# Performance work log

Hardware: AMD Instinct MI355X
Metric: run time of the kernel (lower is better)

The kernel has to match this reference:

```python
import jax, jax.numpy as jnp
import numpy as np

HID, NL, NH, DH, FF = 768, 12, 12, 64, 3072
VOCAB, MAXPOS = 30522, 512
T_ELE, T_ROLE = 17, 7
B, L = 16, 256
LN_EPS = 1e-12


def _layernorm(x, g, b):
    mu = x.mean(-1, keepdims=True)
    var = ((x - mu) ** 2).mean(-1, keepdims=True)
    return (x - mu) / jnp.sqrt(var + LN_EPS) * g + b


def _bert(datas, word_emb, pos_emb, type_emb, emb_ln_g, emb_ln_b,
          Wq, bq, Wk, bk, Wv, bv, Wo, bo, ln1_g, ln1_b,
          W1, b1, W2, b2, ln2_g, ln2_b):
    Bv, Lv = datas.shape
    x = word_emb[datas] + pos_emb[:Lv][None] + type_emb[0][None, None]
    x = _layernorm(x, emb_ln_g, emb_ln_b)
    for i in range(NL):  # loop over fixed layer count, not data dims
        q = (x @ Wq[i] + bq[i]).reshape(Bv, Lv, NH, DH)
        k = (x @ Wk[i] + bk[i]).reshape(Bv, Lv, NH, DH)
        v = (x @ Wv[i] + bv[i]).reshape(Bv, Lv, NH, DH)
        att = jax.nn.softmax(jnp.einsum('bqhd,bkhd->bhqk', q, k) / jnp.sqrt(jnp.float32(DH)), axis=-1)
        ctx = jnp.einsum('bhqk,bkhd->bqhd', att, v).reshape(Bv, Lv, HID)
        x = _layernorm(x + ctx @ Wo[i] + bo[i], ln1_g[i], ln1_b[i])
        h = jax.nn.gelu(x @ W1[i] + b1[i], approximate=False)
        x = _layernorm(x + h @ W2[i] + b2[i], ln2_g[i], ln2_b[i])
    return x


def _crf_llh(em, tags, mask, start, end, trans):
    # torchcrf CRF.forward with batch_first=True, reduction='sum'
    Bv, Lv, T = em.shape
    bidx = jnp.arange(Bv)
    em_t = jnp.transpose(em, (1, 0, 2))        # [L,B,T]
    tags_t = tags.T.astype(jnp.int32)          # [L,B]
    mask_t = mask.T.astype(em.dtype)           # [L,B]
    # numerator: score of gold path
    score = start[tags_t[0]] + em_t[0][bidx, tags_t[0]]
    def num_step(s, xs):
        e_t, tg, tp, m = xs
        return s + m * (trans[tp, tg] + e_t[bidx, tg]), None
    score, _ = jax.lax.scan(num_step, score, (em_t[1:], tags_t[1:], tags_t[:-1], mask_t[1:]))
    last_idx = (mask_t.sum(0) - 1).astype(jnp.int32)
    num = score + end[tags[bidx, last_idx]]
    # denominator: forward algorithm (log-sum-exp semiring)
    alpha = start[None] + em_t[0]              # [B,T]
    def den_step(a, xs):
        e_t, m = xs
        nxt = jax.nn.logsumexp(a[:, :, None] + trans[None] + e_t[:, None, :], axis=1)
        return jnp.where(m[:, None] > 0, nxt, a), None
    alpha, _ = jax.lax.scan(den_step, alpha, (em_t[1:], mask_t[1:]))
    den = jax.nn.logsumexp(alpha + end[None], axis=1)
    return jnp.sum(num - den)


def _crf_decode(em, start, end, trans):
    # torchcrf CRF.decode without mask -> full-length Viterbi
    Bv = em.shape[0]
    bidx = jnp.arange(Bv)
    em_t = jnp.transpose(em, (1, 0, 2))        # [L,B,T]
    alpha = start[None] + em_t[0]
    def fwd(a, e_t):
        sc = a[:, :, None] + trans[None]       # [B,T_prev,T_cur]
        return jnp.max(sc, axis=1) + e_t, jnp.argmax(sc, axis=1)
    alpha, hist = jax.lax.scan(fwd, alpha, em_t[1:])   # hist [L-1,B,T]
    last = jnp.argmax(alpha + end[None], axis=1)
    def back(cur, h):
        prev = h[bidx, cur]
        return prev, prev
    _, ys = jax.lax.scan(back, last, hist, reverse=True)  # ys[t] = tag at pos t
    return jnp.concatenate([ys, last[None]], axis=0).T    # [B,L]


def setup_inputs() -> dict:
    key = jax.random.key(0)
    ks = iter(jax.random.split(key, 64))
    n = lambda shape: jax.random.normal(next(ks), shape, dtype=jnp.float32) * 0.02
    inp = {
        'datas': jax.random.randint(next(ks), (B, L), 0, VOCAB, dtype=jnp.int32),
        'ele_labels': jax.random.randint(next(ks), (B, L), 0, T_ELE, dtype=jnp.int32),
        'role_labels': jax.random.randint(next(ks), (B, L), 0, T_ROLE, dtype=jnp.int32),
        'seq_mask': jnp.ones((B, L), dtype=bool),
        'word_emb': n((VOCAB, HID)), 'pos_emb': n((MAXPOS, HID)), 'type_emb': n((2, HID)),
        'emb_ln_g': jnp.ones((HID,)), 'emb_ln_b': jnp.zeros((HID,)),
        'Wq': n((NL, HID, HID)), 'bq': jnp.zeros((NL, HID)),
        'Wk': n((NL, HID, HID)), 'bk': jnp.zeros((NL, HID)),
        'Wv': n((NL, HID, HID)), 'bv': jnp.zeros((NL, HID)),
        'Wo': n((NL, HID, HID)), 'bo': jnp.zeros((NL, HID)),
        'ln1_g': jnp.ones((NL, HID)), 'ln1_b': jnp.zeros((NL, HID)),
        'W1': n((NL, HID, FF)), 'b1': jnp.zeros((NL, FF)),
        'W2': n((NL, FF, HID)), 'b2': jnp.zeros((NL, HID)),
        'ln2_g': jnp.ones((NL, HID)), 'ln2_b': jnp.zeros((NL, HID)),
        'W_ele': n((HID, T_ELE)), 'b_ele': jnp.zeros((T_ELE,)),
        'W_role': n((HID, T_ROLE)), 'b_role': jnp.zeros((T_ROLE,)),
        'ele_start': n((T_ELE,)), 'ele_end': n((T_ELE,)), 'ele_trans': n((T_ELE, T_ELE)),
        'role_start': n((T_ROLE,)), 'role_end': n((T_ROLE,)), 'role_trans': n((T_ROLE, T_ROLE)),
    }
    return inp


def reference(datas, ele_labels, role_labels, seq_mask,
              word_emb, pos_emb, type_emb, emb_ln_g, emb_ln_b,
              Wq, bq, Wk, bk, Wv, bv, Wo, bo, ln1_g, ln1_b,
              W1, b1, W2, b2, ln2_g, ln2_b,
              W_ele, b_ele, W_role, b_role,
              ele_start, ele_end, ele_trans, role_start, role_end, role_trans):
    wemb = _bert(datas, word_emb, pos_emb, type_emb, emb_ln_g, emb_ln_b,
                 Wq, bq, Wk, bk, Wv, bv, Wo, bo, ln1_g, ln1_b,
                 W1, b1, W2, b2, ln2_g, ln2_b)
    ele_em = wemb @ W_ele + b_ele
    role_em = wemb @ W_role + b_role
    mask = seq_mask.astype(jnp.float32)
    ele_llh = _crf_llh(ele_em, ele_labels, mask, ele_start, ele_end, ele_trans)
    role_llh = _crf_llh(role_em, role_labels, mask, role_start, role_end, role_trans)
    loss = -ele_llh - role_llh
    ele_dec = _crf_decode(ele_em, ele_start, ele_end, ele_trans)
    role_dec = _crf_decode(role_em, role_start, role_end, role_trans)
    return loss, ele_dec, role_dec
```

## Files before the change

### kernel.cpp

```cpp
#include <hip/hip_runtime.h>
#include <stdint.h>
#include <math.h>

typedef _Float16 f16;
typedef _Float16 f16x8 __attribute__((ext_vector_type(8)));
typedef float f32x4 __attribute__((ext_vector_type(4)));

#define LO_SCALE 2048.0f
#define INV_LO_SCALE (1.0f/2048.0f)
#define LOG2E 1.4426950408889634f
#define MFMA16(a, b, c) __builtin_amdgcn_mfma_f32_16x16x32_f16(a, b, c, 0, 0, 0)

__device__ __forceinline__ void split1(float x, f16 &hi, f16 &lo) {
    f16 h = (f16)x;
    hi = h;
    lo = (f16)((x - (float)h) * LO_SCALE);
}

__device__ __forceinline__ float fexp2(float x) {
#if __has_builtin(__builtin_amdgcn_exp2f)
    return __builtin_amdgcn_exp2f(x);
#else
    return exp2f(x);
#endif
}
__device__ __forceinline__ float flog2(float x) {
#if __has_builtin(__builtin_amdgcn_logf)
    return __builtin_amdgcn_logf(x);
#else
    return log2f(x);
#endif
}

#define GLOAD16(g, l) __builtin_amdgcn_global_load_lds( \
    (const __attribute__((address_space(1))) void*)(g), \
    (__attribute__((address_space(3))) void*)(l), 16, 0, 0)

template<int EPI>
__global__ __launch_bounds__(256, 2)
void gemm_split(const f16* __restrict__ Ah, const f16* __restrict__ Al,
                const f16* __restrict__ Bh, const f16* __restrict__ Bl,
                const float* __restrict__ bias, float* __restrict__ C,
                f16* __restrict__ Oh, f16* __restrict__ Ol,
                f16* __restrict__ X2h, f16* __restrict__ X2l,
                f16* __restrict__ X3h, f16* __restrict__ X3l, int K, int N)
{
    __shared__ f16 smem[2][16384];

    const int m0 = blockIdx.x * 128;
    const int n0 = blockIdx.y * 128;
    const int tid = threadIdx.x;
    const int lane = tid & 63;
    const int w = tid >> 6;
    const int wr = (w >> 1) * 64;
    const int wc = (w & 1) * 64;

    f32x4 accm[4][4];
    f32x4 accc[4][4];
#pragma unroll
    for (int i = 0; i < 4; ++i)
#pragma unroll
        for (int j = 0; j < 4; ++j) {
            accm[i][j] = (f32x4){0.f, 0.f, 0.f, 0.f};
            accc[i][j] = (f32x4){0.f, 0.f, 0.f, 0.f};
        }

    const int srow = lane & 15;
    const int skb = lane >> 4;
    const f16* gA0 = Ah + (size_t)(m0 + w * 32 + srow) * K + skb * 8;
    const f16* gA1 = gA0 + 16 * (size_t)K;
    const f16* gCl0 = Al + (size_t)(m0 + w * 32 + srow) * K + skb * 8;
    const f16* gCl1 = gCl0 + 16 * (size_t)K;
    const f16* gB0 = Bh + (size_t)(n0 + w * 32 + srow) * K + skb * 8;
    const f16* gB1 = gB0 + 16 * (size_t)K;
    const f16* gDl0 = Bl + (size_t)(n0 + w * 32 + srow) * K + skb * 8;
    const f16* gDl1 = gDl0 + 16 * (size_t)K;
    const int ldsb0 = w * 1024;
    const int ldsb1 = w * 1024 + 512;

    const int r16 = lane & 15;
    const int kb = lane >> 4;
    const int wrg = (w >> 1) * 4;
    const int wcg = (w & 1) * 4;

    const int nt = K >> 5;

#define STAGE(buf, k0)                                   \
    {                                                    \
        f16* sb = &smem[buf][0];                         \
        GLOAD16(gA0 + (k0), sb + ldsb0);                 \
        GLOAD16(gA1 + (k0), sb + ldsb1);                 \
        GLOAD16(gCl0 + (k0), sb + 4096 + ldsb0);         \
        GLOAD16(gCl1 + (k0), sb + 4096 + ldsb1);         \
        GLOAD16(gB0 + (k0), sb + 8192 + ldsb0);          \
        GLOAD16(gB1 + (k0), sb + 8192 + ldsb1);          \
        GLOAD16(gDl0 + (k0), sb + 12288 + ldsb0);        \
        GLOAD16(gDl1 + (k0), sb + 12288 + ldsb1);        \
    }

    STAGE(0, 0);
    __syncthreads();

    int cur = 0;
    for (int t = 0; t < nt; ++t) {
        if (t + 1 < nt) STAGE(cur ^ 1, (t + 1) * 32);

        const f16* sb = &smem[cur][0];
        f16x8 fah[4], fal[4], fbh[4], fbl[4];
#pragma unroll
        for (int mi = 0; mi < 4; ++mi) {
            int offa = (wrg + mi) * 512 + kb * 128 + r16 * 8;
            fah[mi] = *(const f16x8*)(sb + offa);
            fal[mi] = *(const f16x8*)(sb + 4096 + offa);
            int offb = (wcg + mi) * 512 + kb * 128 + r16 * 8;
            fbh[mi] = *(const f16x8*)(sb + 8192 + offb);
            fbl[mi] = *(const f16x8*)(sb + 12288 + offb);
        }
#pragma unroll
        for (int mi = 0; mi < 4; ++mi)
#pragma unroll
            for (int ni = 0; ni < 4; ++ni) {
                accm[mi][ni] = MFMA16(fah[mi], fbh[ni], accm[mi][ni]);
                accc[mi][ni] = MFMA16(fah[mi], fbl[ni], accc[mi][ni]);
                accc[mi][ni] = MFMA16(fal[mi], fbh[ni], accc[mi][ni]);
            }

        __syncthreads();
        cur ^= 1;
    }
#undef STAGE

#pragma unroll
    for (int mi = 0; mi < 4; ++mi) {
        int row = m0 + wr + mi * 16 + (lane >> 4) * 4;
#pragma unroll
        for (int ni = 0; ni < 4; ++ni) {
            int col = n0 + wc + ni * 16 + (lane & 15);
            float bv = bias[col];
#pragma unroll
            for (int j = 0; j < 4; ++j) {
                float val = accm[mi][ni][j] + accc[mi][ni][j] * INV_LO_SCALE + bv;
                if constexpr (EPI == 0) {
                    C[(size_t)(row + j) * N + col] = val;
                } else if constexpr (EPI == 1) {
                    float ge = 0.5f * val * (1.0f + erff(val * 0.70710678118654752440f));
                    f16 hi, lo;
                    split1(ge, hi, lo);
                    size_t o = (size_t)(row + j) * N + col;
                    Oh[o] = hi;
                    Ol[o] = lo;
                } else {
                    int sect = col >= 1536 ? 2 : (col >= 768 ? 1 : 0);
                    int cc = col - sect * 768;
                    int hd = cc >> 6;
                    int d = cc & 63;
                    int rr = row + j;
                    int bh = (rr >> 8) * 12 + hd;
                    int lt = rr & 255;
                    f16 hi, lo;
                    split1(val, hi, lo);
                    if (sect == 0) {
                        size_t o = ((size_t)bh * 256 + lt) * 64 + d;
                        Oh[o] = hi; Ol[o] = lo;
                    } else if (sect == 1) {
                        size_t o = ((size_t)bh * 256 + lt) * 64 + d;
                        X2h[o] = hi; X2l[o] = lo;
                    } else {
                        size_t o = ((size_t)bh * 64 + d) * 256 + lt;
                        X3h[o] = hi; X3l[o] = lo;
                    }
                }
            }
        }
    }
}

__global__ __launch_bounds__(256, 1)
void attn_mfma_kernel(const f16* __restrict__ Qh, const f16* __restrict__ Ql,
                      const f16* __restrict__ Kh, const f16* __restrict__ Kl,
                      const f16* __restrict__ Vth, const f16* __restrict__ Vtl,
                      f16* __restrict__ ch, f16* __restrict__ cl)
{
    __shared__ f16 sKh[256 * 72];
    __shared__ f16 sKl[256 * 72];
    __shared__ f16 sVh[64 * 264];
    __shared__ f16 sVl[64 * 264];
    __shared__ f16 sPh[4][1280];
    __shared__ f16 sPl[4][1280];

    const int bh = blockIdx.x >> 1;
    const int qbase = (blockIdx.x & 1) * 128;
    const int b = bh / 12;
    const int h = bh % 12;
    const int tid = threadIdx.x;
    const int w = tid >> 6;
    const int l = tid & 63;
    const int l15 = l & 15;
    const int lg = l >> 4;

    {
        const f16* gKh = Kh + (size_t)bh * 16384;
        const f16* gKl = Kl + (size_t)bh * 16384;
#pragma unroll
        for (int i = 0; i < 8; ++i) {
            int c = tid + i * 256;
            int off = (c >> 3) * 72 + (c & 7) * 8;
            *(f16x8*)(sKh + off) = *(const f16x8*)(gKh + c * 8);
            *(f16x8*)(sKl + off) = *(const f16x8*)(gKl + c * 8);
        }
        const f16* gVh = Vth + (size_t)bh * 16384;
        const f16* gVl = Vtl + (size_t)bh * 16384;
#pragma unroll
        for (int i = 0; i < 8; ++i) {
            int c = tid + i * 256;
            int off = (c >> 5) * 264 + (c & 31) * 8;
            *(f16x8*)(sVh + off) = *(const f16x8*)(gVh + c * 8);
            *(f16x8*)(sVl + off) = *(const f16x8*)(gVl + c * 8);
        }
    }
    __syncthreads();

    f16x8 qfh[2][2], qfl[2][2];
#pragma unroll
    for (int mt = 0; mt < 2; ++mt) {
        int qr = qbase + w * 32 + mt * 16 + l15;
        size_t qo = ((size_t)bh * 256 + qr) * 64 + lg * 8;
        qfh[mt][0] = *(const f16x8*)(Qh + qo);
        qfh[mt][1] = *(const f16x8*)(Qh + qo + 32);
        qfl[mt][0] = *(const f16x8*)(Ql + qo);
        qfl[mt][1] = *(const f16x8*)(Ql + qo + 32);
    }

    f32x4 S[2][16];
#pragma unroll
    for (int nt = 0; nt < 16; ++nt) {
        int kr = nt * 16 + l15;
        int kaddr = kr * 72 + lg * 8;
        f16x8 kh0 = *(const f16x8*)(sKh + kaddr);
        f16x8 kh1 = *(const f16x8*)(sKh + kaddr + 32);
        f16x8 kl0 = *(const f16x8*)(sKl + kaddr);
        f16x8 kl1 = *(const f16x8*)(sKl + kaddr + 32);
#pragma unroll
        for (int mt = 0; mt < 2; ++mt) {
            f32x4 am = (f32x4){0.f, 0.f, 0.f, 0.f};
            f32x4 ac = (f32x4){0.f, 0.f, 0.f, 0.f};
            am = MFMA16(qfh[mt][0], kh0, am);
            am = MFMA16(qfh[mt][1], kh1, am);
            ac = MFMA16(qfh[mt][0], kl0, ac);
            ac = MFMA16(qfh[mt][1], kl1, ac);
            ac = MFMA16(qfl[mt][0], kh0, ac);
            ac = MFMA16(qfl[mt][1], kh1, ac);
            S[mt][nt] = (am + ac * INV_LO_SCALE) * 0.125f;
        }
    }

#pragma unroll
    for (int mt = 0; mt < 2; ++mt)
#pragma unroll
        for (int j = 0; j < 4; ++j) {
            float m = S[mt][0][j];
#pragma unroll
            for (int nt = 1; nt < 16; ++nt) m = fmaxf(m, S[mt][nt][j]);
            m = fmaxf(m, __shfl_xor(m, 1));
            m = fmaxf(m, __shfl_xor(m, 2));
            m = fmaxf(m, __shfl_xor(m, 4));
            m = fmaxf(m, __shfl_xor(m, 8));
            float s = 0.f;
#pragma unroll
            for (int nt = 0; nt < 16; ++nt) {
                float e = fexp2((S[mt][nt][j] - m) * LOG2E);
                S[mt][nt][j] = e;
                s += e;
            }
            s += __shfl_xor(s, 1);
            s += __shfl_xor(s, 2);
            s += __shfl_xor(s, 4);
            s += __shfl_xor(s, 8);
            float inv = 1.0f / s;
#pragma unroll
            for (int nt = 0; nt < 16; ++nt) S[mt][nt][j] *= inv;
        }

    f32x4 Ohh[2][4], Occ[2][4];
#pragma unroll
    for (int mt = 0; mt < 2; ++mt)
#pragma unroll
        for (int dt = 0; dt < 4; ++dt) {
            Ohh[mt][dt] = (f32x4){0.f, 0.f, 0.f, 0.f};
            Occ[mt][dt] = (f32x4){0.f, 0.f, 0.f, 0.f};
        }

    f16* pbh = &sPh[w][0];
    f16* pbl = &sPl[w][0];
#pragma unroll
    for (int kp = 0; kp < 8; ++kp) {
#pragma unroll
        for (int mt = 0; mt < 2; ++mt)
#pragma unroll
            for (int n2 = 0; n2 < 2; ++n2) {
                int nt = kp * 2 + n2;
#pragma unroll
                for (int j = 0; j < 4; ++j) {
                    int prow = mt * 16 + lg * 4 + j;
                    int pcol = n2 * 16 + l15;
                    f16 hi, lo;
                    split1(S[mt][nt][j], hi, lo);
                    pbh[prow * 40 + pcol] = hi;
                    pbl[prow * 40 + pcol] = lo;
                }
            }
        __builtin_amdgcn_wave_barrier();
#pragma unroll
        for (int mt = 0; mt < 2; ++mt) {
            int paddr = (mt * 16 + l15) * 40 + lg * 8;
            f16x8 ph = *(const f16x8*)(pbh + paddr);
            f16x8 pl = *(const f16x8*)(pbl + paddr);
#pragma unroll
            for (int dt = 0; dt < 4; ++dt) {
                int vaddr = (dt * 16 + l15) * 264 + kp * 32 + lg * 8;
                f16x8 vh = *(const f16x8*)(sVh + vaddr);
                f16x8 vl = *(const f16x8*)(sVl + vaddr);
                Ohh[mt][dt] = MFMA16(ph, vh, Ohh[mt][dt]);
                Occ[mt][dt] = MFMA16(ph, vl, Occ[mt][dt]);
                Occ[mt][dt] = MFMA16(pl, vh, Occ[mt][dt]);
            }
        }
        __builtin_amdgcn_wave_barrier();
    }

#pragma unroll
    for (int mt = 0; mt < 2; ++mt)
#pragma unroll
        for (int dt = 0; dt < 4; ++dt) {
            f32x4 o = Ohh[mt][dt] + Occ[mt][dt] * INV_LO_SCALE;
#pragma unroll
            for (int j = 0; j < 4; ++j) {
                int q = qbase + w * 32 + mt * 16 + lg * 4 + j;
                int d = dt * 16 + l15;
                size_t off = ((size_t)(b * 256 + q)) * 768 + h * 64 + d;
                f16 hi, lo;
                split1(o[j], hi, lo);
                ch[off] = hi;
                cl[off] = lo;
            }
        }
}

__device__ __forceinline__ void tsplit_tile(const float* __restrict__ W,
                                            f16* __restrict__ Th, f16* __restrict__ Tl,
                                            int K, int N, int kb, int nb, int tid,
                                            float (*tile)[33])
{
    const int k0 = kb * 32;
    const int n0 = nb * 32;
    const int r = tid >> 3;
    const int c4 = (tid & 7) * 4;
    float4 v = *(const float4*)&W[(size_t)(k0 + r) * N + n0 + c4];
    tile[r][c4 + 0] = v.x; tile[r][c4 + 1] = v.y;
    tile[r][c4 + 2] = v.z; tile[r][c4 + 3] = v.w;
    __syncthreads();
    f16 hs[4], ls[4];
#pragma unroll
    for (int j = 0; j < 4; ++j) split1(tile[c4 + j][r], hs[j], ls[j]);
    size_t o = (size_t)(n0 + r) * K + k0 + c4;
    Th[o + 0] = hs[0]; Th[o + 1] = hs[1]; Th[o + 2] = hs[2]; Th[o + 3] = hs[3];
    Tl[o + 0] = ls[0]; Tl[o + 1] = ls[1]; Tl[o + 2] = ls[2]; Tl[o + 3] = ls[3];
}

__global__ void tsplit_all_kernel(const float* __restrict__ Wq, const float* __restrict__ Wk,
                                  const float* __restrict__ Wv, const float* __restrict__ Wo,
                                  const float* __restrict__ W1, const float* __restrict__ W2,
                                  f16* __restrict__ qkvh, f16* __restrict__ qkvl,
                                  f16* __restrict__ woh, f16* __restrict__ wol,
                                  f16* __restrict__ w1h, f16* __restrict__ w1l,
                                  f16* __restrict__ w2h, f16* __restrict__ w2l)
{
    __shared__ float tile[32][33];
    const int tid = threadIdx.x;
    int bid = blockIdx.x;
    if (bid < 576) {
        tsplit_tile(Wq, qkvh, qkvl, 768, 768, bid % 24, bid / 24, tid, tile);
    } else if (bid < 1152) {
        bid -= 576;
        tsplit_tile(Wk, qkvh + 768 * 768, qkvl + 768 * 768, 768, 768, bid % 24, bid / 24, tid, tile);
    } else if (bid < 1728) {
        bid -= 1152;
        tsplit_tile(Wv, qkvh + 2 * 768 * 768, qkvl + 2 * 768 * 768, 768, 768, bid % 24, bid / 24, tid, tile);
    } else if (bid < 2304) {
        bid -= 1728;
        tsplit_tile(Wo, woh, wol, 768, 768, bid % 24, bid / 24, tid, tile);
    } else if (bid < 4608) {
        bid -= 2304;
        tsplit_tile(W1, w1h, w1l, 768, 3072, bid % 24, bid / 24, tid, tile);
    } else {
        bid -= 4608;
        tsplit_tile(W2, w2h, w2l, 3072, 768, bid % 96, bid / 96, tid, tile);
    }
}

__global__ void pack_qkv_bias_kernel(const float* __restrict__ bq, const float* __restrict__ bk,
                                     const float* __restrict__ bv, float* __restrict__ qkvb)
{
    const int i = blockIdx.x;
    const int tid = threadIdx.x;
    for (int c = tid; c < 768; c += 256) {
        qkvb[i * 2304 + c]        = bq[i * 768 + c];
        qkvb[i * 2304 + 768 + c]  = bk[i * 768 + c];
        qkvb[i * 2304 + 1536 + c] = bv[i * 768 + c];
    }
}

__device__ void ln_emit(float* vals, float* red, const float* __restrict__ g,
                        const float* __restrict__ be, float* xout,
                        f16* oh, f16* ol, size_t base, int tid)
{
    float s = vals[tid] + vals[tid + 256] + vals[tid + 512];
    red[tid] = s;
    __syncthreads();
    for (int st = 128; st > 0; st >>= 1) { if (tid < st) red[tid] += red[tid + st]; __syncthreads(); }
    float mu = red[0] * (1.0f / 768.0f);
    __syncthreads();
    float d0 = vals[tid] - mu, d1 = vals[tid + 256] - mu, d2 = vals[tid + 512] - mu;
    red[tid] = d0 * d0 + d1 * d1 + d2 * d2;
    __syncthreads();
    for (int st = 128; st > 0; st >>= 1) { if (tid < st) red[tid] += red[tid + st]; __syncthreads(); }
    float var = red[0] * (1.0f / 768.0f);
    float rstd = 1.0f / sqrtf(var + 1e-12f);
    __syncthreads();
    for (int c = tid; c < 768; c += 256) {
        float o = (vals[c] - mu) * rstd * g[c] + be[c];
        if (xout) xout[base + c] = o;
        f16 hi, lo;
        split1(o, hi, lo);
        oh[base + c] = hi;
        ol[base + c] = lo;
    }
}

__global__ void embed_ln_kernel(const int* __restrict__ datas, const float* __restrict__ wemb,
                                const float* __restrict__ pemb, const float* __restrict__ temb,
                                const float* __restrict__ g, const float* __restrict__ be,
                                float* __restrict__ x, f16* __restrict__ xh, f16* __restrict__ xl)
{
    __shared__ float vals[768];
    __shared__ float red[256];
    const int i = blockIdx.x;
    const int tid = threadIdx.x;
    const int l = i & 255;
    const int widx = datas[i];
    for (int c = tid; c < 768; c += 256)
        vals[c] = wemb[(size_t)widx * 768 + c] + pemb[(size_t)l * 768 + c] + temb[c];
    __syncthreads();
    ln_emit(vals, red, g, be, x, xh, xl, (size_t)i * 768, tid);
}

__global__ void res_ln_kernel(float* __restrict__ x, const float* __restrict__ y,
                              const float* __restrict__ g, const float* __restrict__ be,
                              f16* __restrict__ xh, f16* __restrict__ xl)
{
    __shared__ float vals[768];
    __shared__ float red[256];
    const int i = blockIdx.x;
    const int tid = threadIdx.x;
    const size_t base = (size_t)i * 768;
    for (int c = tid; c < 768; c += 256) vals[c] = x[base + c] + y[base + c];
    __syncthreads();
    ln_emit(vals, red, g, be, x, xh, xl, base, tid);
}

__global__ void head_kernel(const float* __restrict__ X, const float* __restrict__ Wh,
                            const float* __restrict__ bh, float* __restrict__ out, int T)
{
    __shared__ float xs[768];
    __shared__ double part[8][32];
    const int i = blockIdx.x;
    const int tid = threadIdx.x;
    for (int c = tid; c < 768; c += 256) xs[c] = X[(size_t)i * 768 + c];
    __syncthreads();
    const int p = tid >> 5;
    const int tg = tid & 31;
    if (tg < T) {
        double a = 0;
        for (int d = p * 96; d < p * 96 + 96; ++d)
            a += (double)xs[d] * (double)Wh[d * T + tg];
        part[p][tg] = a;
    }
    __syncthreads();
    if (tid < T) {
        double s = 0;
        for (int pp = 0; pp < 8; ++pp) s += part[pp][tid];
        out[(size_t)i * T + tid] = (float)(s + (double)bh[tid]);
    }
}

__global__ void crf_num_kernel(const float* __restrict__ em, const int* __restrict__ labels,
                               const float* __restrict__ start, const float* __restrict__ endv,
                               const float* __restrict__ trans, float* __restrict__ num, int T)
{
    __shared__ double red[256];
    const int b = blockIdx.x;
    const int tid = threadIdx.x;
    const int tag = labels[b * 256 + tid];
    float v;
    if (tid == 0) {
        v = start[tag] + em[(size_t)(b * 256) * T + tag];
    } else {
        int pt = labels[b * 256 + tid - 1];
        v = trans[pt * T + tag] + em[(size_t)(b * 256 + tid) * T + tag];
    }
    red[tid] = (double)v;
    __syncthreads();
    for (int st = 128; st > 0; st >>= 1) { if (tid < st) red[tid] += red[tid + st]; __syncthreads(); }
    if (tid == 0) num[b] = (float)(red[0] + (double)endv[labels[b * 256 + 255]]);
}

template<int T>
__global__ void crf_scan_kernel(const float* __restrict__ emG, const float* __restrict__ start,
                                const float* __restrict__ endv, const float* __restrict__ trans,
                                float* __restrict__ den, float* __restrict__ tagOut)
{
    __shared__ float ems[256 * T];
    __shared__ float albuf[32];
    __shared__ unsigned char hist[255 * T + 1];
    const int b = blockIdx.x;
    const bool vit = (blockIdx.y == 1);
    const int c = threadIdx.x;

    for (int idx = c; idx < 256 * T; idx += 64)
        ems[idx] = emG[(size_t)b * 256 * T + idx];
    float trc[T];
#pragma unroll
    for (int p = 0; p < T; ++p) trc[p] = (c < T) ? trans[p * T + c] : 0.f;
    const float ec = (c < T) ? endv[c] : -1e30f;
    __syncthreads();

    float alpha = (c < T) ? (start[c] + ems[c]) : -1e30f;

    if (!vit) {
        for (int t = 1; t < 256; ++t) {
            if (c < T) albuf[c] = alpha;
            __builtin_amdgcn_wave_barrier();
            float a[T];
            float m = -1e30f;
#pragma unroll
            for (int p = 0; p < T; ++p) { a[p] = albuf[p] + trc[p]; m = fmaxf(m, a[p]); }
            float s = 0.f;
#pragma unroll
            for (int p = 0; p < T; ++p) s += fexp2((a[p] - m) * LOG2E);
            float na = m + flog2(s) * 0.6931471805599453f + ems[t * T + c];
            __builtin_amdgcn_wave_barrier();
            if (c < T) alpha = na;
        }
        if (c < T) albuf[c] = alpha + ec;
        __builtin_amdgcn_wave_barrier();
        if (c == 0) {
            float m = -1e30f;
            for (int p = 0; p < T; ++p) m = fmaxf(m, albuf[p]);
            float s = 0.f;
            for (int p = 0; p < T; ++p) s += fexp2((albuf[p] - m) * LOG2E);
            den[b] = m + flog2(s) * 0.6931471805599453f;
        }
    } else {
        for (int t = 1; t < 256; ++t) {
            if (c < T) albuf[c] = alpha;
            __builtin_amdgcn_wave_barrier();
            float best = albuf[0] + trc[0];
            int arg = 0;
#pragma unroll
            for (int p = 1; p < T; ++p) {
                float v2 = albuf[p] + trc[p];
                if (v2 > best) { best = v2; arg = p; }
            }
            __builtin_amdgcn_wave_barrier();
            if (c < T) {
                alpha = best + ems[t * T + c];
                hist[(t - 1) * T + c] = (unsigned char)arg;
            }
        }
        if (c < T) albuf[c] = alpha + ec;
        __builtin_amdgcn_wave_barrier();
        if (c == 0) {
            float bv = albuf[0];
            int cur = 0;
            for (int p = 1; p < T; ++p) {
                if (albuf[p] > bv) { bv = albuf[p]; cur = p; }
            }
            tagOut[b * 256 + 255] = (float)cur;
            for (int t = 254; t >= 0; --t) {
                cur = hist[t * T + cur];
                tagOut[b * 256 + t] = (float)cur;
            }
        }
    }
}

__global__ void loss_kernel(const float* __restrict__ num, const float* __restrict__ den,
                            float* __restrict__ out)
{
    __shared__ double red[32];
    const int tid = threadIdx.x;
    red[tid] = (double)num[tid] - (double)den[tid];
    __syncthreads();
    for (int st = 16; st > 0; st >>= 1) { if (tid < st) red[tid] += red[tid + st]; __syncthreads(); }
    if (tid == 0) out[0] = (float)(-red[0]);
}

extern "C" void kernel_launch(void* const* d_in, const int* in_sizes, int n_in,
                              void* d_out, int out_size, void* d_ws, size_t ws_size,
                              hipStream_t stream)
{
    (void)in_sizes; (void)n_in; (void)out_size; (void)ws_size;
    const int* datas       = (const int*)d_in[0];
    const int* ele_labels  = (const int*)d_in[1];
    const int* role_labels = (const int*)d_in[2];
    const float* word_emb = (const float*)d_in[4];
    const float* pos_emb  = (const float*)d_in[5];
    const float* type_emb = (const float*)d_in[6];
    const float* emb_g = (const float*)d_in[7];
    const float* emb_b = (const float*)d_in[8];
    const float* Wq = (const float*)d_in[9];  const float* bq = (const float*)d_in[10];
    const float* Wk = (const float*)d_in[11]; const float* bk = (const float*)d_in[12];
    const float* Wv = (const float*)d_in[13]; const float* bv = (const float*)d_in[14];
    const float* Wo = (const float*)d_in[15]; const float* bo = (const float*)d_in[16];
    const float* ln1g = (const float*)d_in[17]; const float* ln1b = (const float*)d_in[18];
    const float* W1 = (const float*)d_in[19]; const float* b1 = (const float*)d_in[20];
    const float* W2 = (const float*)d_in[21]; const float* b2 = (const float*)d_in[22];
    const float* ln2g = (const float*)d_in[23]; const float* ln2b = (const float*)d_in[24];
    const float* W_ele = (const float*)d_in[25]; const float* b_ele = (const float*)d_in[26];
    const float* W_role = (const float*)d_in[27]; const float* b_role = (const float*)d_in[28];
    const float* ele_start = (const float*)d_in[29];
    const float* ele_end   = (const float*)d_in[30];
    const float* ele_trans = (const float*)d_in[31];
    const float* role_start = (const float*)d_in[32];
    const float* role_end   = (const float*)d_in[33];
    const float* role_trans = (const float*)d_in[34];
    float* out = (float*)d_out;

    uint8_t* ws = (uint8_t*)d_ws;
    float* x      = (float*)(ws + 0x0000000);
    f16* xh       = (f16*)  (ws + 0x0C00000);
    f16* xl       = (f16*)  (ws + 0x1200000);
    f16* Qh       = (f16*)  (ws + 0x1800000);
    f16* Ql       = (f16*)  (ws + 0x1E00000);
    f16* Kh       = (f16*)  (ws + 0x2400000);
    f16* Kl       = (f16*)  (ws + 0x2A00000);
    f16* Vth      = (f16*)  (ws + 0x3000000);
    f16* Vtl      = (f16*)  (ws + 0x3600000);
    f16* ctxh     = (f16*)  (ws + 0x3C00000);
    f16* ctxl     = (f16*)  (ws + 0x4200000);
    float* rbuf   = (float*)(ws + 0x4800000);
    f16* hh       = (f16*)  (ws + 0x1800000);
    f16* hl       = (f16*)  (ws + 0x3000000);
    f16* wqkv_h   = (f16*)  (ws + 0x5400000);
    f16* wqkv_l   = (f16*)  (ws + 0x5760000);
    f16* wo_h     = (f16*)  (ws + 0x5AC0000);
    f16* wo_l     = (f16*)  (ws + 0x5BE0000);
    f16* w1_h     = (f16*)  (ws + 0x5D00000);
    f16* w1_l     = (f16*)  (ws + 0x6180000);
    f16* w2_h     = (f16*)  (ws + 0x6600000);
    f16* w2_l     = (f16*)  (ws + 0x6A80000);
    float* qkvb   = (float*)(ws + 0x6F00000);
    float* ele_em = (float*)(ws + 0x6F20000);
    float* role_em= (float*)(ws + 0x6F70000);
    float* numb   = (float*)(ws + 0x6FC0000);
    float* denb   = (float*)(ws + 0x6FC0100);

    pack_qkv_bias_kernel<<<12, 256, 0, stream>>>(bq, bk, bv, qkvb);
    embed_ln_kernel<<<4096, 256, 0, stream>>>(datas, word_emb, pos_emb, type_emb,
                                              emb_g, emb_b, x, xh, xl);

    for (int i = 0; i < 12; ++i) {
        const size_t o768 = (size_t)i * 768 * 768;
        const size_t o3072 = (size_t)i * 768 * 3072;
        tsplit_all_kernel<<<6912, 256, 0, stream>>>(Wq + o768, Wk + o768, Wv + o768, Wo + o768,
                                                    W1 + o3072, W2 + o3072,
                                                    wqkv_h, wqkv_l, wo_h, wo_l,
                                                    w1_h, w1_l, w2_h, w2_l);
        gemm_split<2><<<dim3(32, 18), 256, 0, stream>>>(xh, xl, wqkv_h, wqkv_l,
                                                        qkvb + i * 2304, nullptr,
                                                        Qh, Ql, Kh, Kl, Vth, Vtl, 768, 2304);
        attn_mfma_kernel<<<384, 256, 0, stream>>>(Qh, Ql, Kh, Kl, Vth, Vtl, ctxh, ctxl);
        gemm_split<0><<<dim3(32, 6), 256, 0, stream>>>(ctxh, ctxl, wo_h, wo_l,
                                                       bo + i * 768, rbuf, nullptr, nullptr,
                                                       nullptr, nullptr, nullptr, nullptr, 768, 768);
        res_ln_kernel<<<4096, 256, 0, stream>>>(x, rbuf, ln1g + i * 768, ln1b + i * 768, xh, xl);
        gemm_split<1><<<dim3(32, 24), 256, 0, stream>>>(xh, xl, w1_h, w1_l,
                                                        b1 + i * 3072, nullptr, hh, hl,
                                                        nullptr, nullptr, nullptr, nullptr, 768, 3072);
        gemm_split<0><<<dim3(32, 6), 256, 0, stream>>>(hh, hl, w2_h, w2_l,
                                                       b2 + i * 768, rbuf, nullptr, nullptr,
                                                       nullptr, nullptr, nullptr, nullptr, 3072, 768);
        res_ln_kernel<<<4096, 256, 0, stream>>>(x, rbuf, ln2g + i * 768, ln2b + i * 768, xh, xl);
    }

    head_kernel<<<4096, 256, 0, stream>>>(x, W_ele, b_ele, ele_em, 17);
    head_kernel<<<4096, 256, 0, stream>>>(x, W_role, b_role, role_em, 7);

    crf_num_kernel<<<16, 256, 0, stream>>>(ele_em, ele_labels, ele_start, ele_end, ele_trans, numb, 17);
    crf_num_kernel<<<16, 256, 0, stream>>>(role_em, role_labels, role_start, role_end, role_trans, numb + 16, 7);
    crf_scan_kernel<17><<<dim3(16, 2), 64, 0, stream>>>(ele_em, ele_start, ele_end, ele_trans, denb, out + 1);
    crf_scan_kernel<7><<<dim3(16, 2), 64, 0, stream>>>(role_em, role_start, role_end, role_trans, denb + 16, out + 1 + 4096);
    loss_kernel<<<1, 32, 0, stream>>>(numb, denb, out);
}
```

Baseline: 5.931 ms.

## Add 256x128-tile triple-buffered GEMM for QKV and FFN1 with XCD-aware block remap

Adds a new 512-thread GEMM kernel with a 256x128 output tile, a three-stage LDS ring fed by global_load_lds, staggered prefetch interleaved with the MFMA loop, and s_setprio around the MFMA bursts. It is used for the QKV and FFN-up projections in place of the 128x128 double-buffered kernel, aiming for more operand reuse per block and better hiding of load latency. The existing kernel also gains a blockIdx remap that spreads neighbouring tiles across the eight XCDs for L2 locality. The risks are lower occupancy from the large LDS footprint and one block per CU, and fewer blocks in the grid.

```diff
diff --git a/kernel.cpp b/kernel.cpp
--- a/kernel.cpp
+++ b/kernel.cpp
@@ -35,6 +35,177 @@
 #define GLOAD16(g, l) __builtin_amdgcn_global_load_lds( \
     (const __attribute__((address_space(1))) void*)(g), \
     (__attribute__((address_space(3))) void*)(l), 16, 0, 0)
+
+template<int EPI>
+__device__ __forceinline__ void epi_write(float val, int row, int col, int N,
+                                          float* __restrict__ C,
+                                          f16* __restrict__ Oh, f16* __restrict__ Ol,
+                                          f16* __restrict__ X2h, f16* __restrict__ X2l,
+                                          f16* __restrict__ X3h, f16* __restrict__ X3l)
+{
+    if constexpr (EPI == 0) {
+        C[(size_t)row * N + col] = val;
+    } else if constexpr (EPI == 1) {
+        float ge = 0.5f * val * (1.0f + erff(val * 0.70710678118654752440f));
+        f16 hi, lo;
+        split1(ge, hi, lo);
+        size_t o = (size_t)row * N + col;
+        Oh[o] = hi;
+        Ol[o] = lo;
+    } else {
+        int sect = col >= 1536 ? 2 : (col >= 768 ? 1 : 0);
+        int cc = col - sect * 768;
+        int hd = cc >> 6;
+        int d = cc & 63;
+        int bh = (row >> 8) * 12 + hd;
+        int lt = row & 255;
+        f16 hi, lo;
+        split1(val, hi, lo);
+        if (sect == 0) {
+            size_t o = ((size_t)bh * 256 + lt) * 64 + d;
+            Oh[o] = hi; Ol[o] = lo;
+        } else if (sect == 1) {
+            size_t o = ((size_t)bh * 256 + lt) * 64 + d;
+            X2h[o] = hi; X2l[o] = lo;
+        } else {
+            size_t o = ((size_t)bh * 64 + d) * 256 + lt;
+            X3h[o] = hi; X3l[o] = lo;
+        }
+    }
+}
+
+template<int EPI>
+__global__ __launch_bounds__(512, 1)
+void gemm256(const f16* __restrict__ Ah, const f16* __restrict__ Al,
+             const f16* __restrict__ Bh, const f16* __restrict__ Bl,
+             const float* __restrict__ bias, float* __restrict__ C,
+             f16* __restrict__ Oh, f16* __restrict__ Ol,
+             f16* __restrict__ X2h, f16* __restrict__ X2l,
+             f16* __restrict__ X3h, f16* __restrict__ X3l, int K, int N)
+{
+    __shared__ f16 smem[3][24576];
+
+    const int nwg = (N >> 7) << 4;
+    int s = blockIdx.x + blockIdx.y * 16;
+    const int q = nwg >> 3;
+    int wg = (s & 7) * q + (s >> 3);
+    const int m0 = (wg & 15) * 256;
+    const int n0 = (wg >> 4) * 128;
+
+    const int tid = threadIdx.x;
+    const int w = tid >> 6;
+    const int lane = tid & 63;
+    const int l15 = lane & 15;
+    const int lg = lane >> 4;
+
+    f32x4 accm[4][4];
+    f32x4 accc[4][4];
+#pragma unroll
+    for (int i = 0; i < 4; ++i)
+#pragma unroll
+        for (int j = 0; j < 4; ++j) {
+            accm[i][j] = (f32x4){0.f, 0.f, 0.f, 0.f};
+            accc[i][j] = (f32x4){0.f, 0.f, 0.f, 0.f};
+        }
+
+    const int r0 = m0 + w * 32 + l15;
+    const int c0 = n0 + w * 16 + l15;
+    const f16* gAh0 = Ah + (size_t)r0 * K + lg * 8;
+    const f16* gAh1 = gAh0 + 16 * (size_t)K;
+    const f16* gAl0 = Al + (size_t)r0 * K + lg * 8;
+    const f16* gAl1 = gAl0 + 16 * (size_t)K;
+    const f16* gBh0 = Bh + (size_t)c0 * K + lg * 8;
+    const f16* gBl0 = Bl + (size_t)c0 * K + lg * 8;
+
+    const int nt = K >> 5;
+    const int fro = lg * 128 + l15 * 8;
+
+    {
+        f16* sb = &smem[0][0];
+        GLOAD16(gAh0, sb + w * 1024);
+        GLOAD16(gAl0, sb + 8192 + w * 1024);
+        GLOAD16(gAh1, sb + w * 1024 + 512);
+        GLOAD16(gAl1, sb + 8192 + w * 1024 + 512);
+        GLOAD16(gBh0, sb + 16384 + w * 512);
+        GLOAD16(gBl0, sb + 20480 + w * 512);
+        sb = &smem[1][0];
+        GLOAD16(gAh0 + 32, sb + w * 1024);
+        GLOAD16(gAl0 + 32, sb + 8192 + w * 1024);
+        GLOAD16(gAh1 + 32, sb + w * 1024 + 512);
+        GLOAD16(gAl1 + 32, sb + 8192 + w * 1024 + 512);
+        GLOAD16(gBh0 + 32, sb + 16384 + w * 512);
+        GLOAD16(gBl0 + 32, sb + 20480 + w * 512);
+    }
+
+    int bt = 0;
+    for (int t = 0; t < nt; ++t) {
+        if (t + 1 < nt) {
+            asm volatile("s_waitcnt vmcnt(6)" ::: "memory");
+        } else {
+            asm volatile("s_waitcnt vmcnt(0)" ::: "memory");
+        }
+        __builtin_amdgcn_s_barrier();
+        __builtin_amdgcn_sched_barrier(0);
+
+        const f16* sb = &smem[bt][0];
+        int bs = bt + 2; if (bs >= 3) bs -= 3;
+        f16* sb2 = &smem[bs][0];
+        const bool doStage = (t + 2 < nt);
+        const int k2 = (t + 2) * 32;
+
+        f16x8 fbh[4], fbl[4];
+#pragma unroll
+        for (int ni = 0; ni < 4; ++ni) {
+            int g = (w & 1) * 4 + ni;
+            fbh[ni] = *(const f16x8*)(sb + 16384 + g * 512 + fro);
+            fbl[ni] = *(const f16x8*)(sb + 20480 + g * 512 + fro);
+        }
+#pragma unroll
+        for (int mt = 0; mt < 4; ++mt) {
+            if (doStage) {
+                if (mt == 0) {
+                    GLOAD16(gAh0 + k2, sb2 + w * 1024);
+                    GLOAD16(gAl0 + k2, sb2 + 8192 + w * 1024);
+                } else if (mt == 1) {
+                    GLOAD16(gAh1 + k2, sb2 + w * 1024 + 512);
+                    GLOAD16(gAl1 + k2, sb2 + 8192 + w * 1024 + 512);
+                } else if (mt == 2) {
+                    GLOAD16(gBh0 + k2, sb2 + 16384 + w * 512);
+                    GLOAD16(gBl0 + k2, sb2 + 20480 + w * 512);
+                }
+            }
+            int ga = (w >> 1) * 4 + mt;
+            f16x8 fah = *(const f16x8*)(sb + ga * 512 + fro);
+            f16x8 fal = *(const f16x8*)(sb + 8192 + ga * 512 + fro);
+            __builtin_amdgcn_s_setprio(1);
+#pragma unroll
+            for (int ni = 0; ni < 4; ++ni) {
+                accm[mt][ni] = MFMA16(fah, fbh[ni], accm[mt][ni]);
+                accc[mt][ni] = MFMA16(fah, fbl[ni], accc[mt][ni]);
+                accc[mt][ni] = MFMA16(fal, fbh[ni], accc[mt][ni]);
+            }
+            __builtin_amdgcn_s_setprio(0);
+        }
+        bt = bt + 1; if (bt >= 3) bt = 0;
+    }
+
+    const int wr = (w >> 1) * 64;
+    const int wc = (w & 1) * 64;
+#pragma unroll
+    for (int mt = 0; mt < 4; ++mt) {
+        int row = m0 + wr + mt * 16 + lg * 4;
+#pragma unroll
+        for (int ni = 0; ni < 4; ++ni) {
+            int col = n0 + wc + ni * 16 + l15;
+            float bv = bias[col];
+#pragma unroll
+            for (int j = 0; j < 4; ++j) {
+                float val = accm[mt][ni][j] + accc[mt][ni][j] * INV_LO_SCALE + bv;
+                epi_write<EPI>(val, row + j, col, N, C, Oh, Ol, X2h, X2l, X3h, X3l);
+            }
+        }
+    }
+}
 
 template<int EPI>
 __global__ __launch_bounds__(256, 2)
@@ -47,8 +218,16 @@
 {
     __shared__ f16 smem[2][16384];
 
-    const int m0 = blockIdx.x * 128;
-    const int n0 = blockIdx.y * 128;
+    const int nwg = gridDim.x * gridDim.y;
+    int s = blockIdx.x + blockIdx.y * gridDim.x;
+    int wg = s;
+    if ((nwg & 7) == 0) {
+        int q = nwg >> 3;
+        wg = (s & 7) * q + (s >> 3);
+    }
+    const int m0 = (wg % gridDim.x) * 128;
+    const int n0 = (wg / gridDim.x) * 128;
+
     const int tid = threadIdx.x;
     const int lane = tid & 63;
     const int w = tid >> 6;
@@ -140,36 +319,7 @@
 #pragma unroll
             for (int j = 0; j < 4; ++j) {
                 float val = accm[mi][ni][j] + accc[mi][ni][j] * INV_LO_SCALE + bv;
-                if constexpr (EPI == 0) {
-                    C[(size_t)(row + j) * N + col] = val;
-                } else if constexpr (EPI == 1) {
-                    float ge = 0.5f * val * (1.0f + erff(val * 0.70710678118654752440f));
-                    f16 hi, lo;
-                    split1(ge, hi, lo);
-                    size_t o = (size_t)(row + j) * N + col;
-                    Oh[o] = hi;
-                    Ol[o] = lo;
-                } else {
-                    int sect = col >= 1536 ? 2 : (col >= 768 ? 1 : 0);
-                    int cc = col - sect * 768;
-                    int hd = cc >> 6;
-                    int d = cc & 63;
-                    int rr = row + j;
-                    int bh = (rr >> 8) * 12 + hd;
-                    int lt = rr & 255;
-                    f16 hi, lo;
-                    split1(val, hi, lo);
-                    if (sect == 0) {
-                        size_t o = ((size_t)bh * 256 + lt) * 64 + d;
-                        Oh[o] = hi; Ol[o] = lo;
-                    } else if (sect == 1) {
-                        size_t o = ((size_t)bh * 256 + lt) * 64 + d;
-                        X2h[o] = hi; X2l[o] = lo;
-                    } else {
-                        size_t o = ((size_t)bh * 64 + d) * 256 + lt;
-                        X3h[o] = hi; X3l[o] = lo;
-                    }
-                }
+                epi_write<EPI>(val, row + j, col, N, C, Oh, Ol, X2h, X2l, X3h, X3l);
             }
         }
     }
@@ -676,17 +826,17 @@
                                                     W1 + o3072, W2 + o3072,
                                                     wqkv_h, wqkv_l, wo_h, wo_l,
                                                     w1_h, w1_l, w2_h, w2_l);
-        gemm_split<2><<<dim3(32, 18), 256, 0, stream>>>(xh, xl, wqkv_h, wqkv_l,
-                                                        qkvb + i * 2304, nullptr,
-                                                        Qh, Ql, Kh, Kl, Vth, Vtl, 768, 2304);
+        gemm256<2><<<dim3(16, 18), 512, 0, stream>>>(xh, xl, wqkv_h, wqkv_l,
+                                                     qkvb + i * 2304, nullptr,
+                                                     Qh, Ql, Kh, Kl, Vth, Vtl, 768, 2304);
         attn_mfma_kernel<<<384, 256, 0, stream>>>(Qh, Ql, Kh, Kl, Vth, Vtl, ctxh, ctxl);
         gemm_split<0><<<dim3(32, 6), 256, 0, stream>>>(ctxh, ctxl, wo_h, wo_l,
                                                        bo + i * 768, rbuf, nullptr, nullptr,
                                                        nullptr, nullptr, nullptr, nullptr, 768, 768);
         res_ln_kernel<<<4096, 256, 0, stream>>>(x, rbuf, ln1g + i * 768, ln1b + i * 768, xh, xl);
-        gemm_split<1><<<dim3(32, 24), 256, 0, stream>>>(xh, xl, w1_h, w1_l,
-                                                        b1 + i * 3072, nullptr, hh, hl,
-                                                        nullptr, nullptr, nullptr, nullptr, 768, 3072);
+        gemm256<1><<<dim3(16, 24), 512, 0, stream>>>(xh, xl, w1_h, w1_l,
+                                                     b1 + i * 3072, nullptr, hh, hl,
+                                                     nullptr, nullptr, nullptr, nullptr, 768, 3072);
         gemm_split<0><<<dim3(32, 6), 256, 0, stream>>>(hh, hl, w2_h, w2_l,
                                                        b2 + i * 768, rbuf, nullptr, nullptr,
                                                        nullptr, nullptr, nullptr, nullptr, 3072, 768);
```

Result: slower. 6.059 ms (+2.1%).

## Use 128x64 GEMM tiles with XCD-aware block remap and MFMA priority

Applied to the files above, without the earlier changes.

Replaces the 128x128 split-fp16 GEMM with a 128x64 tile variant that doubles the grid, lowers LDS and register use, and raises the launch-bounds occupancy hint from 2 to 3. Workgroup IDs are remapped so that consecutive tiles land on the same XCD, and s_setprio raises wave priority around the MFMA bursts. The aim is better CU fill and latency hiding on the small-grid Wo/W2 GEMMs. The cost is more A-matrix reloads per output and lower MFMA-to-LDS-load reuse per wave. The remap assumes the block count is divisible by 8.

```diff
diff --git a/kernel.cpp b/kernel.cpp
--- a/kernel.cpp
+++ b/kernel.cpp
@@ -37,139 +37,149 @@
     (__attribute__((address_space(3))) void*)(l), 16, 0, 0)
 
 template<int EPI>
-__global__ __launch_bounds__(256, 2)
-void gemm_split(const f16* __restrict__ Ah, const f16* __restrict__ Al,
-                const f16* __restrict__ Bh, const f16* __restrict__ Bl,
-                const float* __restrict__ bias, float* __restrict__ C,
-                f16* __restrict__ Oh, f16* __restrict__ Ol,
-                f16* __restrict__ X2h, f16* __restrict__ X2l,
-                f16* __restrict__ X3h, f16* __restrict__ X3l, int K, int N)
-{
-    __shared__ f16 smem[2][16384];
-
-    const int m0 = blockIdx.x * 128;
-    const int n0 = blockIdx.y * 128;
+__device__ __forceinline__ void epi_write(float val, int row, int col, int N,
+                                          float* __restrict__ C,
+                                          f16* __restrict__ Oh, f16* __restrict__ Ol,
+                                          f16* __restrict__ X2h, f16* __restrict__ X2l,
+                                          f16* __restrict__ X3h, f16* __restrict__ X3l)
+{
+    if constexpr (EPI == 0) {
+        C[(size_t)row * N + col] = val;
+    } else if constexpr (EPI == 1) {
+        float ge = 0.5f * val * (1.0f + erff(val * 0.70710678118654752440f));
+        f16 hi, lo;
+        split1(ge, hi, lo);
+        size_t o = (size_t)row * N + col;
+        Oh[o] = hi;
+        Ol[o] = lo;
+    } else {
+        int sect = col >= 1536 ? 2 : (col >= 768 ? 1 : 0);
+        int cc = col - sect * 768;
+        int hd = cc >> 6;
+        int d = cc & 63;
+        int bh = (row >> 8) * 12 + hd;
+        int lt = row & 255;
+        f16 hi, lo;
+        split1(val, hi, lo);
+        if (sect == 0) {
+            size_t o = ((size_t)bh * 256 + lt) * 64 + d;
+            Oh[o] = hi; Ol[o] = lo;
+        } else if (sect == 1) {
+            size_t o = ((size_t)bh * 256 + lt) * 64 + d;
+            X2h[o] = hi; X2l[o] = lo;
+        } else {
+            size_t o = ((size_t)bh * 64 + d) * 256 + lt;
+            X3h[o] = hi; X3l[o] = lo;
+        }
+    }
+}
+
+template<int EPI>
+__global__ __launch_bounds__(256, 3)
+void gemm_t64(const f16* __restrict__ Ah, const f16* __restrict__ Al,
+              const f16* __restrict__ Bh, const f16* __restrict__ Bl,
+              const float* __restrict__ bias, float* __restrict__ C,
+              f16* __restrict__ Oh, f16* __restrict__ Ol,
+              f16* __restrict__ X2h, f16* __restrict__ X2l,
+              f16* __restrict__ X3h, f16* __restrict__ X3l, int K, int N)
+{
+    __shared__ f16 smem[2][12288];
+
+    const int nwg = gridDim.x * gridDim.y;
+    int s = blockIdx.x + blockIdx.y * gridDim.x;
+    const int q = nwg >> 3;
+    const int wg = (s & 7) * q + (s >> 3);
+    const int m0 = (wg & 31) * 128;
+    const int n0 = (wg >> 5) * 64;
+
     const int tid = threadIdx.x;
     const int lane = tid & 63;
     const int w = tid >> 6;
-    const int wr = (w >> 1) * 64;
-    const int wc = (w & 1) * 64;
-
-    f32x4 accm[4][4];
-    f32x4 accc[4][4];
+    const int l15 = lane & 15;
+    const int lg = lane >> 4;
+
+    f32x4 accm[4][2];
+    f32x4 accc[4][2];
 #pragma unroll
     for (int i = 0; i < 4; ++i)
 #pragma unroll
-        for (int j = 0; j < 4; ++j) {
+        for (int j = 0; j < 2; ++j) {
             accm[i][j] = (f32x4){0.f, 0.f, 0.f, 0.f};
             accc[i][j] = (f32x4){0.f, 0.f, 0.f, 0.f};
         }
 
-    const int srow = lane & 15;
-    const int skb = lane >> 4;
-    const f16* gA0 = Ah + (size_t)(m0 + w * 32 + srow) * K + skb * 8;
+    const f16* gA0 = Ah + (size_t)(m0 + w * 32 + l15) * K + lg * 8;
     const f16* gA1 = gA0 + 16 * (size_t)K;
-    const f16* gCl0 = Al + (size_t)(m0 + w * 32 + srow) * K + skb * 8;
-    const f16* gCl1 = gCl0 + 16 * (size_t)K;
-    const f16* gB0 = Bh + (size_t)(n0 + w * 32 + srow) * K + skb * 8;
-    const f16* gB1 = gB0 + 16 * (size_t)K;
-    const f16* gDl0 = Bl + (size_t)(n0 + w * 32 + srow) * K + skb * 8;
-    const f16* gDl1 = gDl0 + 16 * (size_t)K;
-    const int ldsb0 = w * 1024;
-    const int ldsb1 = w * 1024 + 512;
-
-    const int r16 = lane & 15;
-    const int kb = lane >> 4;
-    const int wrg = (w >> 1) * 4;
-    const int wcg = (w & 1) * 4;
+    const f16* gAl0 = Al + (size_t)(m0 + w * 32 + l15) * K + lg * 8;
+    const f16* gAl1 = gAl0 + 16 * (size_t)K;
+    const f16* gB0 = Bh + (size_t)(n0 + w * 16 + l15) * K + lg * 8;
+    const f16* gBl0 = Bl + (size_t)(n0 + w * 16 + l15) * K + lg * 8;
 
     const int nt = K >> 5;
 
 #define STAGE(buf, k0)                                   \
     {                                                    \
         f16* sb = &smem[buf][0];                         \
-        GLOAD16(gA0 + (k0), sb + ldsb0);                 \
-        GLOAD16(gA1 + (k0), sb + ldsb1);                 \
-        GLOAD16(gCl0 + (k0), sb + 4096 + ldsb0);         \
-        GLOAD16(gCl1 + (k0), sb + 4096 + ldsb1);         \
-        GLOAD16(gB0 + (k0), sb + 8192 + ldsb0);          \
-        GLOAD16(gB1 + (k0), sb + 8192 + ldsb1);          \
-        GLOAD16(gDl0 + (k0), sb + 12288 + ldsb0);        \
-        GLOAD16(gDl1 + (k0), sb + 12288 + ldsb1);        \
+        GLOAD16(gA0 + (k0), sb + w * 1024);              \
+        GLOAD16(gA1 + (k0), sb + w * 1024 + 512);        \
+        GLOAD16(gAl0 + (k0), sb + 4096 + w * 1024);      \
+        GLOAD16(gAl1 + (k0), sb + 4096 + w * 1024 + 512);\
+        GLOAD16(gB0 + (k0), sb + 8192 + w * 512);        \
+        GLOAD16(gBl0 + (k0), sb + 10240 + w * 512);      \
     }
 
     STAGE(0, 0);
     __syncthreads();
+
+    const int fro = lg * 128 + l15 * 8;
+    const int wrg = (w >> 1) * 4;
+    const int wcg = (w & 1) * 2;
 
     int cur = 0;
     for (int t = 0; t < nt; ++t) {
         if (t + 1 < nt) STAGE(cur ^ 1, (t + 1) * 32);
 
         const f16* sb = &smem[cur][0];
-        f16x8 fah[4], fal[4], fbh[4], fbl[4];
+        f16x8 fbh[2], fbl[2];
+#pragma unroll
+        for (int ni = 0; ni < 2; ++ni) {
+            int offb = 8192 + (wcg + ni) * 512 + fro;
+            fbh[ni] = *(const f16x8*)(sb + offb);
+            fbl[ni] = *(const f16x8*)(sb + offb + 2048);
+        }
 #pragma unroll
         for (int mi = 0; mi < 4; ++mi) {
-            int offa = (wrg + mi) * 512 + kb * 128 + r16 * 8;
-            fah[mi] = *(const f16x8*)(sb + offa);
-            fal[mi] = *(const f16x8*)(sb + 4096 + offa);
-            int offb = (wcg + mi) * 512 + kb * 128 + r16 * 8;
-            fbh[mi] = *(const f16x8*)(sb + 8192 + offb);
-            fbl[mi] = *(const f16x8*)(sb + 12288 + offb);
-        }
-#pragma unroll
-        for (int mi = 0; mi < 4; ++mi)
-#pragma unroll
-            for (int ni = 0; ni < 4; ++ni) {
-                accm[mi][ni] = MFMA16(fah[mi], fbh[ni], accm[mi][ni]);
-                accc[mi][ni] = MFMA16(fah[mi], fbl[ni], accc[mi][ni]);
-                accc[mi][ni] = MFMA16(fal[mi], fbh[ni], accc[mi][ni]);
-            }
+            int offa = (wrg + mi) * 512 + fro;
+            f16x8 fah = *(const f16x8*)(sb + offa);
+            f16x8 fal = *(const f16x8*)(sb + offa + 4096);
+            __builtin_amdgcn_s_setprio(1);
+#pragma unroll
+            for (int ni = 0; ni < 2; ++ni) {
+                accm[mi][ni] = MFMA16(fah, fbh[ni], accm[mi][ni]);
+                accc[mi][ni] = MFMA16(fah, fbl[ni], accc[mi][ni]);
+                accc[mi][ni] = MFMA16(fal, fbh[ni], accc[mi][ni]);
+            }
+            __builtin_amdgcn_s_setprio(0);
+        }
 
         __syncthreads();
         cur ^= 1;
     }
 #undef STAGE
 
+    const int wr = (w >> 1) * 64;
+    const int wc = (w & 1) * 32;
 #pragma unroll
     for (int mi = 0; mi < 4; ++mi) {
-        int row = m0 + wr + mi * 16 + (lane >> 4) * 4;
-#pragma unroll
-        for (int ni = 0; ni < 4; ++ni) {
-            int col = n0 + wc + ni * 16 + (lane & 15);
+        int row = m0 + wr + mi * 16 + lg * 4;
+#pragma unroll
+        for (int ni = 0; ni < 2; ++ni) {
+            int col = n0 + wc + ni * 16 + l15;
             float bv = bias[col];
 #pragma unroll
             for (int j = 0; j < 4; ++j) {
                 float val = accm[mi][ni][j] + accc[mi][ni][j] * INV_LO_SCALE + bv;
-                if constexpr (EPI == 0) {
-                    C[(size_t)(row + j) * N + col] = val;
-                } else if constexpr (EPI == 1) {
-                    float ge = 0.5f * val * (1.0f + erff(val * 0.70710678118654752440f));
-                    f16 hi, lo;
-                    split1(ge, hi, lo);
-                    size_t o = (size_t)(row + j) * N + col;
-                    Oh[o] = hi;
-                    Ol[o] = lo;
-                } else {
-                    int sect = col >= 1536 ? 2 : (col >= 768 ? 1 : 0);
-                    int cc = col - sect * 768;
-                    int hd = cc >> 6;
-                    int d = cc & 63;
-                    int rr = row + j;
-                    int bh = (rr >> 8) * 12 + hd;
-                    int lt = rr & 255;
-                    f16 hi, lo;
-                    split1(val, hi, lo);
-                    if (sect == 0) {
-                        size_t o = ((size_t)bh * 256 + lt) * 64 + d;
-                        Oh[o] = hi; Ol[o] = lo;
-                    } else if (sect == 1) {
-                        size_t o = ((size_t)bh * 256 + lt) * 64 + d;
-                        X2h[o] = hi; X2l[o] = lo;
-                    } else {
-                        size_t o = ((size_t)bh * 64 + d) * 256 + lt;
-                        X3h[o] = hi; X3l[o] = lo;
-                    }
-                }
+                epi_write<EPI>(val, row + j, col, N, C, Oh, Ol, X2h, X2l, X3h, X3l);
             }
         }
     }
@@ -676,20 +686,20 @@
                                                     W1 + o3072, W2 + o3072,
                                                     wqkv_h, wqkv_l, wo_h, wo_l,
                                                     w1_h, w1_l, w2_h, w2_l);
-        gemm_split<2><<<dim3(32, 18), 256, 0, stream>>>(xh, xl, wqkv_h, wqkv_l,
-                                                        qkvb + i * 2304, nullptr,
-                                                        Qh, Ql, Kh, Kl, Vth, Vtl, 768, 2304);
+        gemm_t64<2><<<dim3(32, 36), 256, 0, stream>>>(xh, xl, wqkv_h, wqkv_l,
+                                                      qkvb + i * 2304, nullptr,
+                                                      Qh, Ql, Kh, Kl, Vth, Vtl, 768, 2304);
         attn_mfma_kernel<<<384, 256, 0, stream>>>(Qh, Ql, Kh, Kl, Vth, Vtl, ctxh, ctxl);
-        gemm_split<0><<<dim3(32, 6), 256, 0, stream>>>(ctxh, ctxl, wo_h, wo_l,
-                                                       bo + i * 768, rbuf, nullptr, nullptr,
-                                                       nullptr, nullptr, nullptr, nullptr, 768, 768);
+        gemm_t64<0><<<dim3(32, 12), 256, 0, stream>>>(ctxh, ctxl, wo_h, wo_l,
+                                                      bo + i * 768, rbuf, nullptr, nullptr,
+                                                      nullptr, nullptr, nullptr, nullptr, 768, 768);
         res_ln_kernel<<<4096, 256, 0, stream>>>(x, rbuf, ln1g + i * 768, ln1b + i * 768, xh, xl);
-        gemm_split<1><<<dim3(32, 24), 256, 0, stream>>>(xh, xl, w1_h, w1_l,
-                                                        b1 + i * 3072, nullptr, hh, hl,
-                                                        nullptr, nullptr, nullptr, nullptr, 768, 3072);
-        gemm_split<0><<<dim3(32, 6), 256, 0, stream>>>(hh, hl, w2_h, w2_l,
-                                                       b2 + i * 768, rbuf, nullptr, nullptr,
-                                                       nullptr, nullptr, nullptr, nullptr, 3072, 768);
+        gemm_t64<1><<<dim3(32, 48), 256, 0, stream>>>(xh, xl, w1_h, w1_l,
+                                                      b1 + i * 3072, nullptr, hh, hl,
+                                                      nullptr, nullptr, nullptr, nullptr, 768, 3072);
+        gemm_t64<0><<<dim3(32, 12), 256, 0, stream>>>(hh, hl, w2_h, w2_l,
+                                                      b2 + i * 768, rbuf, nullptr, nullptr,
+                                                      nullptr, nullptr, nullptr, nullptr, 3072, 768);
         res_ln_kernel<<<4096, 256, 0, stream>>>(x, rbuf, ln2g + i * 768, ln2b + i * 768, xh, xl);
     }
 
```

After: 6.012 ms. Within noise of the previous version (+1.4%).
